# Performance work log

Measured on AMD Instinct MI355X. Metric: run time of the kernel, lower is better.

## Reference

```python
import jax, jax.numpy as jnp
import numpy as np

EMBED, VOCAB, NUM_DIGEST, EXPAND = 128, 50257, 4, 4


def _mueller_hash(k):
    # https://stackoverflow.com/a/12996028 , uint32 wraparound semantics
    k = (k >> np.uint32(16) ^ k) * np.uint32(73244475)
    k = (k >> np.uint32(16) ^ k) * np.uint32(73244475)
    k = k >> np.uint32(16) ^ k
    return k


def setup_inputs() -> dict:
    key = jax.random.key(0)
    k_tok, k_tab, k_w1, k_w2 = jax.random.split(key, 4)
    # bloom ledger hash indices (exact replication of bloom_ledger)
    ids = np.arange(VOCAB, dtype=np.uint32)
    i_list, j_list = [], []
    for _ in range(NUM_DIGEST):
        ids = _mueller_hash(ids)
        i_list.append(ids % VOCAB)
        ids = _mueller_hash(ids)
        j_list.append(ids % VOCAB)
    bloom_i = jnp.asarray(np.concatenate(i_list).astype(np.int32))
    bloom_j = jnp.asarray(np.concatenate(j_list).astype(np.int32))
    hidden = EMBED * EXPAND
    return {
        "tokens": jax.random.randint(k_tok, (8, 4096), 0, VOCAB, dtype=jnp.int32),
        "table": jax.random.normal(k_tab, (VOCAB, EMBED), jnp.float32) / np.sqrt(EMBED),
        "bloom_i": bloom_i,
        "bloom_j": bloom_j,
        "w1": jax.random.normal(k_w1, (EMBED, hidden), jnp.float32) / np.sqrt(EMBED),
        "b1": jnp.zeros((hidden,), jnp.float32),
        "w2": jax.random.normal(k_w2, (hidden, EMBED), jnp.float32) / np.sqrt(hidden),
        "b2": jnp.zeros((EMBED,), jnp.float32),
    }


def reference(tokens, table, bloom_i, bloom_j, w1, b1, w2, b2):
    vocab = table.shape[0]
    num_digest = bloom_i.shape[0] // vocab
    scale = jnp.asarray(1.0 / np.sqrt(num_digest), table.dtype)
    # bloom @ table as a scatter-add: A[i] += scale * table[j]  -> [vocab, embed]
    agg = jnp.zeros_like(table).at[bloom_i].add(scale * table[bloom_j])
    # one_hot(tokens) @ (bloom @ table) == row gather
    x = agg[tokens]                      # [B, S, embed]
    h = jax.nn.gelu(x @ w1 + b1)         # [B, S, hidden]
    return h @ w2 + b2                   # [B, S, embed]
```

## Files before the change

### kernel.cpp

```cpp
#include <hip/hip_runtime.h>
#include <hip/hip_bf16.h>
#include <stdint.h>

#define EMBED  128
#define HIDDEN 512
#define TB     32
#define HHALF  256
#define CAP    32

typedef __attribute__((ext_vector_type(8))) short short8v;
typedef __attribute__((ext_vector_type(8))) ushort ushort8v;
typedef __attribute__((ext_vector_type(4))) float f32x4;

__device__ __forceinline__ ushort f2bf(float f) {
    uint32_t b = __float_as_uint(f);
    uint32_t r = (b + 0x7FFFu + ((b >> 16) & 1u)) >> 16;
    return (ushort)r;
}
__device__ __forceinline__ float bf2f(ushort u) {
    return __uint_as_float(((uint32_t)u) << 16);
}

__device__ __forceinline__ float gelu_fast(float x) {
    float x2 = x * x;
    float u  = x * fmaf(0.035677408136f, x2, 0.7978845608f);
    float t  = __expf(2.0f * u);
    return x - x * __frcp_rn(t + 1.0f);
}

__global__ __launch_bounds__(256)
void prep_kernel(const float* __restrict__ w1, const float* __restrict__ w2,
                 ushort* __restrict__ W1t, ushort* __restrict__ W2t,
                 int* __restrict__ cnt, int vocab,
                 const float* __restrict__ table, ushort* __restrict__ tbf,
                 int zb, int n8) {
    __shared__ float T[32][33];
    int b = blockIdx.x;
    int t = threadIdx.x;
    if (b < 128) {
        const float* in; ushort* outp; int inCols, outCols, tr, tc;
        if (b < 64) {
            in = w1; outp = W1t; inCols = 512; outCols = 128;
            tr = b >> 4; tc = b & 15;
        } else {
            int b2 = b - 64;
            in = w2; outp = W2t; inCols = 128; outCols = 512;
            tr = b2 >> 2; tc = b2 & 3;
        }
        int r  = t >> 3;
        int c4 = (t & 7) * 4;
        float4 v = *(const float4*)&in[(size_t)(tr * 32 + r) * inCols + tc * 32 + c4];
        T[c4 + 0][r] = v.x; T[c4 + 1][r] = v.y; T[c4 + 2][r] = v.z; T[c4 + 3][r] = v.w;
        __syncthreads();
        ushort o[4];
        #pragma unroll
        for (int i = 0; i < 4; ++i) o[i] = f2bf(T[r][c4 + i]);
        *(ushort4*)&outp[(size_t)(tc * 32 + r) * outCols + tr * 32 + c4] = *(ushort4*)o;
    } else if (b < 128 + zb) {
        int i = (b - 128) * 256 + t;
        if (i < vocab) cnt[i] = 0;
    } else {
        int gid = (b - 128 - zb) * 256 + t;
        if (gid < n8) {
            const float* src = table + (size_t)gid * 8;
            float4 v0 = *(const float4*)(src);
            float4 v1 = *(const float4*)(src + 4);
            ushort u[8] = {f2bf(v0.x), f2bf(v0.y), f2bf(v0.z), f2bf(v0.w),
                           f2bf(v1.x), f2bf(v1.y), f2bf(v1.z), f2bf(v1.w)};
            *(short8v*)&tbf[(size_t)gid * 8] = *(short8v*)u;
        }
    }
}

__global__ __launch_bounds__(256)
void bucket_kernel(const int* __restrict__ bi, const int* __restrict__ bj,
                   int* __restrict__ cnt, ushort* __restrict__ csr, int nk) {
    int k = blockIdx.x * blockDim.x + threadIdx.x;
    if (k >= nk) return;
    int i = bi[k];
    int slot = atomicAdd(&cnt[i], 1);
    if (slot < CAP) csr[(size_t)i * CAP + slot] = (ushort)bj[k];
}

__global__ __launch_bounds__(512, 6)
void mlp_mfma_kernel(const int*    __restrict__ tokens,
                     const ushort* __restrict__ tbf,
                     const int*    __restrict__ cnt,
                     const ushort* __restrict__ csr,
                     const ushort* __restrict__ W1t,
                     const ushort* __restrict__ W2t,
                     const float*  __restrict__ b1,
                     const float*  __restrict__ b2,
                     float*        __restrict__ out) {
    __shared__ ushort Xs[TB * EMBED];
    __shared__ ushort Hs[TB * HHALF];

    const int t    = threadIdx.x;
    const int lane = t & 63;
    const int wv   = t >> 6;
    const int base = blockIdx.x * TB;
    const int l15  = lane & 15;
    const int lhi  = lane >> 4;

    {
        int r   = t >> 4;
        int c8  = t & 15;
        int tok = tokens[base + r];
        int m   = min(cnt[tok], CAP);
        const ushort* jrow = csr + (size_t)tok * CAP;
        ushort8v jv = *(const ushort8v*)jrow;

        short8v v[8];
        #pragma unroll
        for (int e = 0; e < 8; ++e) {
            int j = (e < m) ? (int)jv[e] : 0;
            v[e] = *(const short8v*)&tbf[(size_t)j * EMBED + c8 * 8];
        }
        float acc[8] = {0.f,0.f,0.f,0.f,0.f,0.f,0.f,0.f};
        #pragma unroll
        for (int e = 0; e < 8; ++e) {
            if (e < m) {
                #pragma unroll
                for (int q = 0; q < 8; ++q) acc[q] += bf2f((ushort)v[e][q]);
            }
        }
        for (int e = 8; e < m; ++e) {
            int j = (int)jrow[e];
            short8v w = *(const short8v*)&tbf[(size_t)j * EMBED + c8 * 8];
            #pragma unroll
            for (int q = 0; q < 8; ++q) acc[q] += bf2f((ushort)w[q]);
        }
        ushort u[8];
        #pragma unroll
        for (int q = 0; q < 8; ++q) u[q] = f2bf(0.5f * acc[q]);
        *(short8v*)&Xs[r * EMBED + (c8 ^ (r & 7)) * 8] = *(short8v*)u;
    }
    __syncthreads();

    f32x4 acc2[2];
    {
        float bv = b2[wv * 16 + l15];
        acc2[0] = (f32x4){bv, bv, bv, bv};
        acc2[1] = acc2[0];
    }

    #pragma unroll
    for (int h = 0; h < 2; ++h) {
        f32x4 acc1[2][2];
        #pragma unroll
        for (int n = 0; n < 2; ++n) {
            float bv = b1[h * HHALF + wv * 32 + n * 16 + l15];
            acc1[0][n] = (f32x4){bv, bv, bv, bv};
            acc1[1][n] = acc1[0][n];
        }
        #pragma unroll
        for (int kk = 0; kk < EMBED / 32; ++kk) {
            short8v a[2];
            #pragma unroll
            for (int m = 0; m < 2; ++m) {
                int r = m * 16 + l15;
                int g = (kk * 4 + lhi) ^ (r & 7);
                a[m] = *(const short8v*)&Xs[r * EMBED + g * 8];
            }
            #pragma unroll
            for (int n = 0; n < 2; ++n) {
                int col = h * HHALF + wv * 32 + n * 16 + l15;
                short8v b = *(const short8v*)(W1t + (size_t)col * EMBED + kk * 32 + lhi * 8);
                #pragma unroll
                for (int m = 0; m < 2; ++m)
                    acc1[m][n] = __builtin_amdgcn_mfma_f32_16x16x32_bf16(a[m], b, acc1[m][n], 0, 0, 0);
            }
        }

        #pragma unroll
        for (int n = 0; n < 2; ++n) {
            int colh = wv * 32 + n * 16 + l15;
            #pragma unroll
            for (int m = 0; m < 2; ++m)
                #pragma unroll
                for (int q = 0; q < 4; ++q) {
                    int row = m * 16 + lhi * 4 + q;
                    float hv = gelu_fast(acc1[m][n][q]);
                    int g = (colh >> 3) ^ (row & 7);
                    Hs[row * HHALF + g * 8 + (colh & 7)] = f2bf(hv);
                }
        }
        __syncthreads();

        #pragma unroll
        for (int kk = 0; kk < HHALF / 32; ++kk) {
            short8v a[2];
            #pragma unroll
            for (int m = 0; m < 2; ++m) {
                int r = m * 16 + l15;
                int g = (kk * 4 + lhi) ^ (r & 7);
                a[m] = *(const short8v*)&Hs[r * HHALF + g * 8];
            }
            int col = wv * 16 + l15;
            short8v b = *(const short8v*)(W2t + (size_t)col * HIDDEN + h * HHALF + kk * 32 + lhi * 8);
            #pragma unroll
            for (int m = 0; m < 2; ++m)
                acc2[m] = __builtin_amdgcn_mfma_f32_16x16x32_bf16(a[m], b, acc2[m], 0, 0, 0);
        }
        __syncthreads();
    }

    #pragma unroll
    for (int m = 0; m < 2; ++m)
        #pragma unroll
        for (int q = 0; q < 4; ++q) {
            int row = m * 16 + lhi * 4 + q;
            out[(size_t)(base + row) * EMBED + wv * 16 + l15] = acc2[m][q];
        }
}

extern "C" void kernel_launch(void* const* d_in, const int* in_sizes, int n_in,
                              void* d_out, int out_size, void* d_ws, size_t ws_size,
                              hipStream_t stream) {
    const int*   tokens = (const int*)  d_in[0];
    const float* table  = (const float*)d_in[1];
    const int*   bi     = (const int*)  d_in[2];
    const int*   bj     = (const int*)  d_in[3];
    const float* w1     = (const float*)d_in[4];
    const float* b1     = (const float*)d_in[5];
    const float* w2     = (const float*)d_in[6];
    const float* b2     = (const float*)d_in[7];
    float* out = (float*)d_out;

    const int vocab = in_sizes[1] / EMBED;
    const int nk    = in_sizes[2];
    const int ntok  = in_sizes[0];

    char* ws = (char*)d_ws;
    size_t off = 0;
    auto alloc = [&](size_t b) { size_t o = off; off += (b + 255) & ~(size_t)255; return o; };
    ushort* W1t = (ushort*)(ws + alloc((size_t)EMBED * HIDDEN * 2));
    ushort* W2t = (ushort*)(ws + alloc((size_t)EMBED * HIDDEN * 2));
    ushort* tbf = (ushort*)(ws + alloc((size_t)vocab * EMBED * 2));
    ushort* csr = (ushort*)(ws + alloc((size_t)vocab * CAP * 2));
    int*    cnt = (int*)   (ws + alloc((size_t)vocab * 4));

    int zb = (vocab + 255) / 256;
    int n8 = vocab * EMBED / 8;
    int cb = (n8 + 255) / 256;
    prep_kernel<<<128 + zb + cb, 256, 0, stream>>>(w1, w2, W1t, W2t, cnt, vocab,
                                                   table, tbf, zb, n8);

    bucket_kernel<<<(nk + 255) / 256, 256, 0, stream>>>(bi, bj, cnt, csr, nk);

    mlp_mfma_kernel<<<ntok / TB, 512, 0, stream>>>(tokens, tbf, cnt, csr,
                                                   W1t, W2t, b1, b2, out);
}
```

Measured before the change: 71.86 us.

## Double token tile to 64 rows and fuse bucket scatter into prep kernel

```diff
diff --git a/kernel.cpp b/kernel.cpp
--- a/kernel.cpp
+++ b/kernel.cpp
@@ -4,7 +4,7 @@
 
 #define EMBED  128
 #define HIDDEN 512
-#define TB     32
+#define TB     64
 #define HHALF  256
 #define CAP    32
 
@@ -28,12 +28,17 @@
     return x - x * __frcp_rn(t + 1.0f);
 }
 
+__global__ void zero_kernel(int* __restrict__ p, int n) {
+    int i = blockIdx.x * blockDim.x + threadIdx.x;
+    if (i < n) p[i] = 0;
+}
+
 __global__ __launch_bounds__(256)
 void prep_kernel(const float* __restrict__ w1, const float* __restrict__ w2,
                  ushort* __restrict__ W1t, ushort* __restrict__ W2t,
-                 int* __restrict__ cnt, int vocab,
-                 const float* __restrict__ table, ushort* __restrict__ tbf,
-                 int zb, int n8) {
+                 const float* __restrict__ table, ushort* __restrict__ tbf, int n8, int cb,
+                 const int* __restrict__ bi, const int* __restrict__ bj, int nk,
+                 int* __restrict__ cnt, ushort* __restrict__ csr) {
     __shared__ float T[32][33];
     int b = blockIdx.x;
     int t = threadIdx.x;
@@ -56,11 +61,8 @@
         #pragma unroll
         for (int i = 0; i < 4; ++i) o[i] = f2bf(T[r][c4 + i]);
         *(ushort4*)&outp[(size_t)(tc * 32 + r) * outCols + tr * 32 + c4] = *(ushort4*)o;
-    } else if (b < 128 + zb) {
-        int i = (b - 128) * 256 + t;
-        if (i < vocab) cnt[i] = 0;
-    } else {
-        int gid = (b - 128 - zb) * 256 + t;
+    } else if (b < 128 + cb) {
+        int gid = (b - 128) * 256 + t;
         if (gid < n8) {
             const float* src = table + (size_t)gid * 8;
             float4 v0 = *(const float4*)(src);
@@ -69,20 +71,17 @@
                            f2bf(v1.x), f2bf(v1.y), f2bf(v1.z), f2bf(v1.w)};
             *(short8v*)&tbf[(size_t)gid * 8] = *(short8v*)u;
         }
-    }
-}
-
-__global__ __launch_bounds__(256)
-void bucket_kernel(const int* __restrict__ bi, const int* __restrict__ bj,
-                   int* __restrict__ cnt, ushort* __restrict__ csr, int nk) {
-    int k = blockIdx.x * blockDim.x + threadIdx.x;
-    if (k >= nk) return;
-    int i = bi[k];
-    int slot = atomicAdd(&cnt[i], 1);
-    if (slot < CAP) csr[(size_t)i * CAP + slot] = (ushort)bj[k];
-}
-
-__global__ __launch_bounds__(512, 6)
+    } else {
+        int k = (b - 128 - cb) * 256 + t;
+        if (k < nk) {
+            int i = bi[k];
+            int slot = atomicAdd(&cnt[i], 1);
+            if (slot < CAP) csr[(size_t)i * CAP + slot] = (ushort)bj[k];
+        }
+    }
+}
+
+__global__ __launch_bounds__(512)
 void mlp_mfma_kernel(const int*    __restrict__ tokens,
                      const ushort* __restrict__ tbf,
                      const int*    __restrict__ cnt,
@@ -103,61 +102,75 @@
     const int lhi  = lane >> 4;
 
     {
-        int r   = t >> 4;
-        int c8  = t & 15;
-        int tok = tokens[base + r];
-        int m   = min(cnt[tok], CAP);
+        int r    = t >> 3;
+        int c16  = t & 7;
+        int tok  = tokens[base + r];
+        int m    = min(cnt[tok], CAP);
         const ushort* jrow = csr + (size_t)tok * CAP;
         ushort8v jv = *(const ushort8v*)jrow;
 
-        short8v v[8];
+        short8v v[8][2];
         #pragma unroll
         for (int e = 0; e < 8; ++e) {
             int j = (e < m) ? (int)jv[e] : 0;
-            v[e] = *(const short8v*)&tbf[(size_t)j * EMBED + c8 * 8];
-        }
-        float acc[8] = {0.f,0.f,0.f,0.f,0.f,0.f,0.f,0.f};
+            const ushort* trp = tbf + (size_t)j * EMBED + c16 * 16;
+            v[e][0] = *(const short8v*)(trp);
+            v[e][1] = *(const short8v*)(trp + 8);
+        }
+        float acc[16] = {0.f,0.f,0.f,0.f,0.f,0.f,0.f,0.f,
+                         0.f,0.f,0.f,0.f,0.f,0.f,0.f,0.f};
         #pragma unroll
         for (int e = 0; e < 8; ++e) {
             if (e < m) {
                 #pragma unroll
-                for (int q = 0; q < 8; ++q) acc[q] += bf2f((ushort)v[e][q]);
+                for (int q = 0; q < 8; ++q) {
+                    acc[q]     += bf2f((ushort)v[e][0][q]);
+                    acc[8 + q] += bf2f((ushort)v[e][1][q]);
+                }
             }
         }
         for (int e = 8; e < m; ++e) {
             int j = (int)jrow[e];
-            short8v w = *(const short8v*)&tbf[(size_t)j * EMBED + c8 * 8];
-            #pragma unroll
-            for (int q = 0; q < 8; ++q) acc[q] += bf2f((ushort)w[q]);
-        }
-        ushort u[8];
-        #pragma unroll
-        for (int q = 0; q < 8; ++q) u[q] = f2bf(0.5f * acc[q]);
-        *(short8v*)&Xs[r * EMBED + (c8 ^ (r & 7)) * 8] = *(short8v*)u;
+            const ushort* trp = tbf + (size_t)j * EMBED + c16 * 16;
+            short8v w0 = *(const short8v*)(trp);
+            short8v w1 = *(const short8v*)(trp + 8);
+            #pragma unroll
+            for (int q = 0; q < 8; ++q) {
+                acc[q]     += bf2f((ushort)w0[q]);
+                acc[8 + q] += bf2f((ushort)w1[q]);
+            }
+        }
+        ushort u[16];
+        #pragma unroll
+        for (int q = 0; q < 16; ++q) u[q] = f2bf(0.5f * acc[q]);
+        int g0 = c16 * 2;
+        #pragma unroll
+        for (int h = 0; h < 2; ++h)
+            *(short8v*)&Xs[r * EMBED + ((g0 + h) ^ (r & 7)) * 8] = *(short8v*)&u[h * 8];
     }
     __syncthreads();
 
-    f32x4 acc2[2];
+    f32x4 acc2[4];
     {
         float bv = b2[wv * 16 + l15];
-        acc2[0] = (f32x4){bv, bv, bv, bv};
-        acc2[1] = acc2[0];
+        #pragma unroll
+        for (int m = 0; m < 4; ++m) acc2[m] = (f32x4){bv, bv, bv, bv};
     }
 
     #pragma unroll
     for (int h = 0; h < 2; ++h) {
-        f32x4 acc1[2][2];
+        f32x4 acc1[4][2];
         #pragma unroll
         for (int n = 0; n < 2; ++n) {
             float bv = b1[h * HHALF + wv * 32 + n * 16 + l15];
-            acc1[0][n] = (f32x4){bv, bv, bv, bv};
-            acc1[1][n] = acc1[0][n];
+            #pragma unroll
+            for (int m = 0; m < 4; ++m) acc1[m][n] = (f32x4){bv, bv, bv, bv};
         }
         #pragma unroll
         for (int kk = 0; kk < EMBED / 32; ++kk) {
-            short8v a[2];
-            #pragma unroll
-            for (int m = 0; m < 2; ++m) {
+            short8v a[4];
+            #pragma unroll
+            for (int m = 0; m < 4; ++m) {
                 int r = m * 16 + l15;
                 int g = (kk * 4 + lhi) ^ (r & 7);
                 a[m] = *(const short8v*)&Xs[r * EMBED + g * 8];
@@ -167,7 +180,7 @@
                 int col = h * HHALF + wv * 32 + n * 16 + l15;
                 short8v b = *(const short8v*)(W1t + (size_t)col * EMBED + kk * 32 + lhi * 8);
                 #pragma unroll
-                for (int m = 0; m < 2; ++m)
+                for (int m = 0; m < 4; ++m)
                     acc1[m][n] = __builtin_amdgcn_mfma_f32_16x16x32_bf16(a[m], b, acc1[m][n], 0, 0, 0);
             }
         }
@@ -176,7 +189,7 @@
         for (int n = 0; n < 2; ++n) {
             int colh = wv * 32 + n * 16 + l15;
             #pragma unroll
-            for (int m = 0; m < 2; ++m)
+            for (int m = 0; m < 4; ++m)
                 #pragma unroll
                 for (int q = 0; q < 4; ++q) {
                     int row = m * 16 + lhi * 4 + q;
@@ -189,9 +202,9 @@
 
         #pragma unroll
         for (int kk = 0; kk < HHALF / 32; ++kk) {
-            short8v a[2];
-            #pragma unroll
-            for (int m = 0; m < 2; ++m) {
+            short8v a[4];
+            #pragma unroll
+            for (int m = 0; m < 4; ++m) {
                 int r = m * 16 + l15;
                 int g = (kk * 4 + lhi) ^ (r & 7);
                 a[m] = *(const short8v*)&Hs[r * HHALF + g * 8];
@@ -199,14 +212,14 @@
             int col = wv * 16 + l15;
             short8v b = *(const short8v*)(W2t + (size_t)col * HIDDEN + h * HHALF + kk * 32 + lhi * 8);
             #pragma unroll
-            for (int m = 0; m < 2; ++m)
+            for (int m = 0; m < 4; ++m)
                 acc2[m] = __builtin_amdgcn_mfma_f32_16x16x32_bf16(a[m], b, acc2[m], 0, 0, 0);
         }
         __syncthreads();
     }
 
     #pragma unroll
-    for (int m = 0; m < 2; ++m)
+    for (int m = 0; m < 4; ++m)
         #pragma unroll
         for (int q = 0; q < 4; ++q) {
             int row = m * 16 + lhi * 4 + q;
@@ -240,13 +253,14 @@
     ushort* csr = (ushort*)(ws + alloc((size_t)vocab * CAP * 2));
     int*    cnt = (int*)   (ws + alloc((size_t)vocab * 4));
 
-    int zb = (vocab + 255) / 256;
+    zero_kernel<<<(vocab + 255) / 256, 256, 0, stream>>>(cnt, vocab);
+
     int n8 = vocab * EMBED / 8;
     int cb = (n8 + 255) / 256;
-    prep_kernel<<<128 + zb + cb, 256, 0, stream>>>(w1, w2, W1t, W2t, cnt, vocab,
-                                                   table, tbf, zb, n8);
-
-    bucket_kernel<<<(nk + 255) / 256, 256, 0, stream>>>(bi, bj, cnt, csr, nk);
+    int bb = (nk + 255) / 256;
+    prep_kernel<<<128 + cb + bb, 256, 0, stream>>>(w1, w2, W1t, W2t,
+                                                   table, tbf, n8, cb,
+                                                   bi, bj, nk, cnt, csr);
 
     mlp_mfma_kernel<<<ntok / TB, 512, 0, stream>>>(tokens, tbf, cnt, csr,
                                                    W1t, W2t, b1, b2, out);
```

New measurement: 58.47 us. -18.6%, faster.

## Process 64 tokens per block over the full hidden width; fold bucketing into prep

Applied to the files above, without the earlier changes.

```diff
diff --git a/kernel.cpp b/kernel.cpp
--- a/kernel.cpp
+++ b/kernel.cpp
@@ -4,8 +4,7 @@
 
 #define EMBED  128
 #define HIDDEN 512
-#define TB     32
-#define HHALF  256
+#define TB     64
 #define CAP    32
 
 typedef __attribute__((ext_vector_type(8))) short short8v;
@@ -28,12 +27,17 @@
     return x - x * __frcp_rn(t + 1.0f);
 }
 
+__global__ void zero_kernel(int* __restrict__ p, int n) {
+    int i = blockIdx.x * blockDim.x + threadIdx.x;
+    if (i < n) p[i] = 0;
+}
+
 __global__ __launch_bounds__(256)
 void prep_kernel(const float* __restrict__ w1, const float* __restrict__ w2,
                  ushort* __restrict__ W1t, ushort* __restrict__ W2t,
-                 int* __restrict__ cnt, int vocab,
-                 const float* __restrict__ table, ushort* __restrict__ tbf,
-                 int zb, int n8) {
+                 const float* __restrict__ table, ushort* __restrict__ tbf, int n8, int cb,
+                 const int* __restrict__ bi, const int* __restrict__ bj, int nk,
+                 int* __restrict__ cnt, ushort* __restrict__ csr) {
     __shared__ float T[32][33];
     int b = blockIdx.x;
     int t = threadIdx.x;
@@ -56,11 +60,8 @@
         #pragma unroll
         for (int i = 0; i < 4; ++i) o[i] = f2bf(T[r][c4 + i]);
         *(ushort4*)&outp[(size_t)(tc * 32 + r) * outCols + tr * 32 + c4] = *(ushort4*)o;
-    } else if (b < 128 + zb) {
-        int i = (b - 128) * 256 + t;
-        if (i < vocab) cnt[i] = 0;
-    } else {
-        int gid = (b - 128 - zb) * 256 + t;
+    } else if (b < 128 + cb) {
+        int gid = (b - 128) * 256 + t;
         if (gid < n8) {
             const float* src = table + (size_t)gid * 8;
             float4 v0 = *(const float4*)(src);
@@ -69,20 +70,17 @@
                            f2bf(v1.x), f2bf(v1.y), f2bf(v1.z), f2bf(v1.w)};
             *(short8v*)&tbf[(size_t)gid * 8] = *(short8v*)u;
         }
-    }
-}
-
-__global__ __launch_bounds__(256)
-void bucket_kernel(const int* __restrict__ bi, const int* __restrict__ bj,
-                   int* __restrict__ cnt, ushort* __restrict__ csr, int nk) {
-    int k = blockIdx.x * blockDim.x + threadIdx.x;
-    if (k >= nk) return;
-    int i = bi[k];
-    int slot = atomicAdd(&cnt[i], 1);
-    if (slot < CAP) csr[(size_t)i * CAP + slot] = (ushort)bj[k];
-}
-
-__global__ __launch_bounds__(512, 6)
+    } else {
+        int k = (b - 128 - cb) * 256 + t;
+        if (k < nk) {
+            int i = bi[k];
+            int slot = atomicAdd(&cnt[i], 1);
+            if (slot < CAP) csr[(size_t)i * CAP + slot] = (ushort)bj[k];
+        }
+    }
+}
+
+__global__ __launch_bounds__(1024, 8)
 void mlp_mfma_kernel(const int*    __restrict__ tokens,
                      const ushort* __restrict__ tbf,
                      const int*    __restrict__ cnt,
@@ -93,7 +91,7 @@
                      const float*  __restrict__ b2,
                      float*        __restrict__ out) {
     __shared__ ushort Xs[TB * EMBED];
-    __shared__ ushort Hs[TB * HHALF];
+    __shared__ ushort Hs[TB * HIDDEN];
 
     const int t    = threadIdx.x;
     const int lane = t & 63;
@@ -137,80 +135,76 @@
     }
     __syncthreads();
 
+    f32x4 acc1[4][2];
+    #pragma unroll
+    for (int n = 0; n < 2; ++n) {
+        float bv = b1[wv * 32 + n * 16 + l15];
+        #pragma unroll
+        for (int m = 0; m < 4; ++m) acc1[m][n] = (f32x4){bv, bv, bv, bv};
+    }
+    #pragma unroll
+    for (int kk = 0; kk < EMBED / 32; ++kk) {
+        short8v a[4];
+        #pragma unroll
+        for (int m = 0; m < 4; ++m) {
+            int r = m * 16 + l15;
+            int g = (kk * 4 + lhi) ^ (r & 7);
+            a[m] = *(const short8v*)&Xs[r * EMBED + g * 8];
+        }
+        #pragma unroll
+        for (int n = 0; n < 2; ++n) {
+            int col = wv * 32 + n * 16 + l15;
+            short8v b = *(const short8v*)(W1t + (size_t)col * EMBED + kk * 32 + lhi * 8);
+            #pragma unroll
+            for (int m = 0; m < 4; ++m)
+                acc1[m][n] = __builtin_amdgcn_mfma_f32_16x16x32_bf16(a[m], b, acc1[m][n], 0, 0, 0);
+        }
+    }
+
+    #pragma unroll
+    for (int n = 0; n < 2; ++n) {
+        int col = wv * 32 + n * 16 + l15;
+        #pragma unroll
+        for (int m = 0; m < 4; ++m)
+            #pragma unroll
+            for (int q = 0; q < 4; ++q) {
+                int row = m * 16 + lhi * 4 + q;
+                float hv = gelu_fast(acc1[m][n][q]);
+                int g = (col >> 3) ^ (row & 7);
+                Hs[row * HIDDEN + g * 8 + (col & 7)] = f2bf(hv);
+            }
+    }
+    __syncthreads();
+
+    const int mh = wv >> 3;
+    const int nc = (wv & 7) * 16;
     f32x4 acc2[2];
     {
-        float bv = b2[wv * 16 + l15];
+        float bv = b2[nc + l15];
         acc2[0] = (f32x4){bv, bv, bv, bv};
         acc2[1] = acc2[0];
     }
-
-    #pragma unroll
-    for (int h = 0; h < 2; ++h) {
-        f32x4 acc1[2][2];
-        #pragma unroll
-        for (int n = 0; n < 2; ++n) {
-            float bv = b1[h * HHALF + wv * 32 + n * 16 + l15];
-            acc1[0][n] = (f32x4){bv, bv, bv, bv};
-            acc1[1][n] = acc1[0][n];
-        }
-        #pragma unroll
-        for (int kk = 0; kk < EMBED / 32; ++kk) {
-            short8v a[2];
-            #pragma unroll
-            for (int m = 0; m < 2; ++m) {
-                int r = m * 16 + l15;
-                int g = (kk * 4 + lhi) ^ (r & 7);
-                a[m] = *(const short8v*)&Xs[r * EMBED + g * 8];
-            }
-            #pragma unroll
-            for (int n = 0; n < 2; ++n) {
-                int col = h * HHALF + wv * 32 + n * 16 + l15;
-                short8v b = *(const short8v*)(W1t + (size_t)col * EMBED + kk * 32 + lhi * 8);
-                #pragma unroll
-                for (int m = 0; m < 2; ++m)
-                    acc1[m][n] = __builtin_amdgcn_mfma_f32_16x16x32_bf16(a[m], b, acc1[m][n], 0, 0, 0);
-            }
-        }
-
-        #pragma unroll
-        for (int n = 0; n < 2; ++n) {
-            int colh = wv * 32 + n * 16 + l15;
-            #pragma unroll
-            for (int m = 0; m < 2; ++m)
-                #pragma unroll
-                for (int q = 0; q < 4; ++q) {
-                    int row = m * 16 + lhi * 4 + q;
-                    float hv = gelu_fast(acc1[m][n][q]);
-                    int g = (colh >> 3) ^ (row & 7);
-                    Hs[row * HHALF + g * 8 + (colh & 7)] = f2bf(hv);
-                }
-        }
-        __syncthreads();
-
-        #pragma unroll
-        for (int kk = 0; kk < HHALF / 32; ++kk) {
-            short8v a[2];
-            #pragma unroll
-            for (int m = 0; m < 2; ++m) {
-                int r = m * 16 + l15;
-                int g = (kk * 4 + lhi) ^ (r & 7);
-                a[m] = *(const short8v*)&Hs[r * HHALF + g * 8];
-            }
-            int col = wv * 16 + l15;
-            short8v b = *(const short8v*)(W2t + (size_t)col * HIDDEN + h * HHALF + kk * 32 + lhi * 8);
-            #pragma unroll
-            for (int m = 0; m < 2; ++m)
-                acc2[m] = __builtin_amdgcn_mfma_f32_16x16x32_bf16(a[m], b, acc2[m], 0, 0, 0);
-        }
-        __syncthreads();
-    }
-
-    #pragma unroll
-    for (int m = 0; m < 2; ++m)
+    #pragma unroll
+    for (int kk = 0; kk < HIDDEN / 32; ++kk) {
+        short8v a[2];
+        #pragma unroll
+        for (int mt = 0; mt < 2; ++mt) {
+            int r = mh * 32 + mt * 16 + l15;
+            int g = (kk * 4 + lhi) ^ (r & 7);
+            a[mt] = *(const short8v*)&Hs[r * HIDDEN + g * 8];
+        }
+        short8v b = *(const short8v*)(W2t + (size_t)(nc + l15) * HIDDEN + kk * 32 + lhi * 8);
+        #pragma unroll
+        for (int mt = 0; mt < 2; ++mt)
+            acc2[mt] = __builtin_amdgcn_mfma_f32_16x16x32_bf16(a[mt], b, acc2[mt], 0, 0, 0);
+    }
+
+    #pragma unroll
+    for (int mt = 0; mt < 2; ++mt)
         #pragma unroll
         for (int q = 0; q < 4; ++q) {
-            int row = m * 16 + lhi * 4 + q;
-            out[(size_t)(base + row) * EMBED + wv * 16 + l15] = acc2[m][q];
+            int row = mh * 32 + mt * 16 + lhi * 4 + q;
+            out[(size_t)(base + row) * EMBED + nc + l15] = acc2[mt][q];
         }
 }
 
@@ -240,14 +234,15 @@
     ushort* csr = (ushort*)(ws + alloc((size_t)vocab * CAP * 2));
     int*    cnt = (int*)   (ws + alloc((size_t)vocab * 4));
 
-    int zb = (vocab + 255) / 256;
+    zero_kernel<<<(vocab + 255) / 256, 256, 0, stream>>>(cnt, vocab);
+
     int n8 = vocab * EMBED / 8;
     int cb = (n8 + 255) / 256;
-    prep_kernel<<<128 + zb + cb, 256, 0, stream>>>(w1, w2, W1t, W2t, cnt, vocab,
-                                                   table, tbf, zb, n8);
-
-    bucket_kernel<<<(nk + 255) / 256, 256, 0, stream>>>(bi, bj, cnt, csr, nk);
-
-    mlp_mfma_kernel<<<ntok / TB, 512, 0, stream>>>(tokens, tbf, cnt, csr,
-                                                   W1t, W2t, b1, b2, out);
-}
+    int bb = (nk + 255) / 256;
+    prep_kernel<<<128 + cb + bb, 256, 0, stream>>>(w1, w2, W1t, W2t,
+                                                   table, tbf, n8, cb,
+                                                   bi, bj, nk, cnt, csr);
+
+    mlp_mfma_kernel<<<ntok / TB, 1024, 0, stream>>>(tokens, tbf, cnt, csr,
+                                                    W1t, W2t, b1, b2, out);
+}
```

Result: slower. 77.10 us (+7.3%).
